# Performance work log

Hardware: AMD Instinct MI355X
Metric: run time of the kernel (lower is better)

## Reference

```python
import jax, jax.numpy as jnp
import numpy as np

N_HEADS = 12
HIDDEN = 768
HEAD_DIM = HIDDEN // N_HEADS
B, S = 4, 2048


def setup_inputs() -> dict:
    key = jax.random.key(0)
    ks = jax.random.split(key, 7)
    bound = 1.0 / np.sqrt(HIDDEN)  # torch nn.Linear default init range
    inputs = jax.random.normal(ks[0], (B, S, HIDDEN), dtype=jnp.float32)
    Wq = jax.random.uniform(ks[1], (HIDDEN, HIDDEN), jnp.float32, -bound, bound)
    bq = jax.random.uniform(ks[2], (HIDDEN,), jnp.float32, -bound, bound)
    Wk = jax.random.uniform(ks[3], (HIDDEN, HIDDEN), jnp.float32, -bound, bound)
    bk = jax.random.uniform(ks[4], (HIDDEN,), jnp.float32, -bound, bound)
    Wv = jax.random.uniform(ks[5], (HIDDEN, HIDDEN), jnp.float32, -bound, bound)
    bv = jax.random.uniform(ks[6], (HIDDEN,), jnp.float32, -bound, bound)
    return {"inputs": inputs, "Wq": Wq, "bq": bq, "Wk": Wk, "bk": bk, "Wv": Wv, "bv": bv}


def reference(inputs, Wq, bq, Wk, bk, Wv, bv):
    b, s, d = inputs.shape
    h, hd = N_HEADS, HEAD_DIM
    # torch Linear: x @ W^T + b; reshape to (b, s, h, hd) -> (b, h, s, hd)
    def proj(W, bias):
        y = inputs @ W.T + bias
        return y.reshape(b, s, h, hd).transpose(0, 2, 1, 3)
    q = proj(Wq, bq)
    k = proj(Wk, bk)
    v = proj(Wv, bv)
    scale = 1.0 / jnp.sqrt(jnp.asarray(hd, inputs.dtype))
    scores = jnp.einsum('bhqd,bhkd->bhqk', q, k) * scale  # [b,h,s,s] materialized as in source
    attn = jax.nn.softmax(scores, axis=-1)
    out = jnp.einsum('bhqk,bhkd->bhqd', attn, v)
    # (b, h, s, hd) -> (b, s, h*hd)
    return out.transpose(0, 2, 1, 3).reshape(b, s, d)
```

## Files before the change

kernel.cpp:

```cpp
#include <hip/hip_runtime.h>
#include <hip/hip_bf16.h>
#include <math.h>

#define NH   12
#define HD   64
#define HID  768
#define NB   4
#define SS   2048
#define MR   (NB*SS)

#define NXE  (MR*HID)
#define NWE  (HID*HID)

typedef unsigned short u16;
typedef u16   u16x8  __attribute__((ext_vector_type(8)));
typedef __bf16 bf16x8 __attribute__((ext_vector_type(8)));
typedef float f32x4  __attribute__((ext_vector_type(4)));

__device__ __forceinline__ u16 f2b(float f) {
    union { float f; unsigned i; } c; c.f = f;
    unsigned x = c.i + 0x7fffu + ((c.i >> 16) & 1u);
    return (u16)(x >> 16);
}
__device__ __forceinline__ unsigned pk2(float lo, float hi) {
    float2 f; f.x = lo; f.y = hi;
    union { __hip_bfloat162 h; unsigned u; } c;
    c.h = __float22bfloat162_rn(f);
    return c.u;
}
__device__ __forceinline__ f32x4 mfma16(u16x8 a, u16x8 b, f32x4 c) {
    return __builtin_amdgcn_mfma_f32_16x16x32_bf16(
        __builtin_bit_cast(bf16x8, a), __builtin_bit_cast(bf16x8, b), c, 0, 0, 0);
}
__device__ __forceinline__ void g2l16(const u16* g, u16* l) {
    __builtin_amdgcn_global_load_lds(
        (const __attribute__((address_space(1))) void*)g,
        (__attribute__((address_space(3))) void*)l, 16, 0, 0);
}
__device__ __forceinline__ int kperm(int k) {
    return ((k >> 5) << 5) | (((k >> 2) & 1) << 4) | (((k >> 3) & 3) << 2) | (k & 3);
}


__global__ __launch_bounds__(256) void to_bf16(
    const float* __restrict__ x,  const float* __restrict__ Wq,
    const float* __restrict__ Wk, const float* __restrict__ Wv,
    u16* __restrict__ dst)
{
    const int NX4 = NXE / 4, NW4 = NWE / 4, NT4 = NX4 + 3 * NW4;
    for (int i = blockIdx.x * 256 + threadIdx.x; i < NT4; i += gridDim.x * 256) {
        const float* src; u16* d;
        if (i < NX4) { src = x + (size_t)i * 4; d = dst + (size_t)i * 4; }
        else {
            int j = i - NX4; int w = j / NW4; int r = j - w * NW4;
            const float* Ws = (w == 0) ? Wq : ((w == 1) ? Wk : Wv);
            src = Ws + (size_t)r * 4; d = dst + NXE + (size_t)w * NWE + (size_t)r * 4;
        }
        float4 f = *(const float4*)src;
        uint2 o; o.x = pk2(f.x, f.y); o.y = pk2(f.z, f.w);
        *(uint2*)d = o;
    }
}

__global__ __launch_bounds__(256, 3) void qkv_proj(
    const u16* __restrict__ xb, const u16* __restrict__ Wb,
    const float* __restrict__ bq, const float* __restrict__ bk,
    const float* __restrict__ bv, u16* __restrict__ qkv)
{
    const int wsel = blockIdx.z;
    const u16* W = Wb + (size_t)wsel * NWE;
    const float* bias = (wsel == 0) ? bq : ((wsel == 1) ? bk : bv);
    u16* out = qkv + (size_t)wsel * MR * HID;

    const int m0 = blockIdx.x * 128, n0 = blockIdx.y * 128;
    __shared__ __align__(16) u16 smem[18432];

    const int tid  = threadIdx.x;
    const int lane = tid & 63, wid = tid >> 6;
    const int quad = lane >> 4, l16 = lane & 15;
    const int wm = wid >> 1, wn = wid & 1;
    const int qsw = quad ^ ((l16 >> 1) & 3);

    const int rA = 2 * wid * 16 + (lane >> 2);
    const int colh = 8 * ((lane & 3) ^ ((lane >> 3) & 3));
    const u16* gx0 = xb + (size_t)(m0 + rA) * HID + colh;
    const u16* gx1 = gx0 + (size_t)16 * HID;
    const u16* gw0 = W  + (size_t)(n0 + rA) * HID + colh;
    const u16* gw1 = gw0 + (size_t)16 * HID;
    u16* lA = smem + (2 * wid) * 512 + lane * 8;

    f32x4 acc[4][4] = {};

    for (int k0 = 0; k0 < HID; k0 += 64) {
        g2l16(gx0 + k0,      lA);            g2l16(gx1 + k0,      lA + 512);
        g2l16(gx0 + k0 + 32, lA + 4096);     g2l16(gx1 + k0 + 32, lA + 4608);
        g2l16(gw0 + k0,      lA + 8192);     g2l16(gw1 + k0,      lA + 8704);
        g2l16(gw0 + k0 + 32, lA + 12288);    g2l16(gw1 + k0 + 32, lA + 12800);
        __syncthreads();
        #pragma unroll
        for (int hh = 0; hh < 2; hh++) {
            u16x8 af[4], bf[4];
            #pragma unroll
            for (int i = 0; i < 4; i++)
                af[i] = *(const u16x8*)(smem + hh * 4096 + (wm * 64 + i * 16 + l16) * 32 + qsw * 8);
            #pragma unroll
            for (int j = 0; j < 4; j++)
                bf[j] = *(const u16x8*)(smem + 8192 + hh * 4096 + (wn * 64 + j * 16 + l16) * 32 + qsw * 8);
            #pragma unroll
            for (int i = 0; i < 4; i++)
                #pragma unroll
                for (int j = 0; j < 4; j++)
                    acc[i][j] = mfma16(af[i], bf[j], acc[i][j]);
        }
        __syncthreads();
    }

    u16* lt = smem + wid * 4608;

    if (wsel == 2) {
        #pragma unroll
        for (int j = 0; j < 4; j++) {
            const int col = n0 + wn * 64 + j * 16 + l16;
            const float bb = bias[col];
            #pragma unroll
            for (int i = 0; i < 4; i++) {
                uint2 pk;
                pk.x = pk2(acc[i][j][0] + bb, acc[i][j][1] + bb);
                pk.y = pk2(acc[i][j][2] + bb, acc[i][j][3] + bb);
                *(uint2*)(lt + (j * 16 + l16) * 72 + i * 16 + quad * 4) = pk;
            }
        }
        __syncthreads();
        const int bidx = m0 >> 11;
        const int s0 = (m0 & 2047) + wm * 64;
        #pragma unroll
        for (int it = 0; it < 8; it++) {
            const int dl = it * 8 + (lane >> 3), sl = (lane & 7) * 8;
            uint4 w = *(const uint4*)(lt + dl * 72 + sl);
            const int col = n0 + wn * 64 + dl;
            const int hh = col >> 6, d = col & 63;
            *(uint4*)(out + ((size_t)(bidx * NH + hh) * HD + d) * SS + s0 + sl) = w;
        }
    } else {
        const float scale = (wsel == 0) ? 0.18033688f : 1.0f;
        #pragma unroll
        for (int j = 0; j < 4; j++) {
            const int col = n0 + wn * 64 + j * 16 + l16;
            const float bb = bias[col];
            #pragma unroll
            for (int i = 0; i < 4; i++)
                #pragma unroll
                for (int r = 0; r < 4; r++)
                    lt[(i * 16 + quad * 4 + r) * 72 + j * 16 + l16] =
                        f2b((acc[i][j][r] + bb) * scale);
        }
        __syncthreads();
        const size_t rowbase = (size_t)(m0 + wm * 64);
        const int cb = n0 + wn * 64;
        #pragma unroll
        for (int it = 0; it < 8; it++) {
            const int dl = it * 8 + (lane >> 3), sl = (lane & 7) * 8;
            uint4 w = *(const uint4*)(lt + dl * 72 + sl);
            const int grow = (wsel == 1) ? kperm(dl) : dl;
            *(uint4*)(out + (rowbase + grow) * HID + cb + sl) = w;
        }
    }
}

__global__ __launch_bounds__(256, 3) void attn(
    const u16* __restrict__ qkv, float* __restrict__ out)
{
    const int lin = blockIdx.x;
    const int rx  = lin & 7;
    const int gg  = lin >> 3;
    const int qt  = gg & 15;
    const int bh  = rx * 6 + (gg >> 4);
    const int b   = bh / NH, h = bh - b * NH;
    const int q0  = qt * 128;

    const u16* qb  = qkv + (size_t)b * SS * HID + h * HD;
    const u16* kb  = qkv + (size_t)MR * HID + (size_t)b * SS * HID + h * HD;
    const u16* vtb = qkv + (size_t)2 * MR * HID + ((size_t)(b * NH + h) * HD) * SS;
    float*     ob  = out + (size_t)b * SS * HID + h * HD;

    __shared__ __align__(16) u16 KS[3][2][2048];
    __shared__ __align__(16) u16 VS[3][2][2048];

    const int tid  = threadIdx.x;
    const int lane = tid & 63, wid = tid >> 6;
    const int quad = lane >> 4, l16 = lane & 15;
    const int qsw = quad ^ ((l16 >> 1) & 3);

    const int srow = 16 * wid + (lane >> 2);
    const int sc8  = 8 * ((lane & 3) ^ ((lane >> 3) & 3));
    const int ldst = wid * 512 + lane * 8;

    const u16* kg = kb + (size_t)srow * HID + sc8;
    const u16* vg = vtb + (size_t)srow * SS + sc8;

#define ASTAGE(kt, bf_) do {                                            \
        const u16* k_ = kg + (size_t)(kt) * 64 * HID;                   \
        const u16* v_ = vg + (kt) * 64;                                 \
        g2l16(k_,      &KS[(bf_)][0][0] + ldst);                        \
        g2l16(k_ + 32, &KS[(bf_)][1][0] + ldst);                        \
        g2l16(v_,      &VS[(bf_)][0][0] + ldst);                        \
        g2l16(v_ + 32, &VS[(bf_)][1][0] + ldst);                        \
    } while (0)

    u16x8 qf[2][2];
    #pragma unroll
    for (int t = 0; t < 2; t++) {
        const int row = q0 + t * 64 + wid * 16 + l16;
        #pragma unroll
        for (int hh = 0; hh < 2; hh++)
            qf[t][hh] = *(const u16x8*)(qb + (size_t)row * HID + hh * 32 + quad * 8);
    }

    u16x8 ones;
    #pragma unroll
    for (int e = 0; e < 8; e++) ones[e] = 0x3F80;

    f32x4 o2[2][4] = {};
    f32x4 lacc[2] = {};

    ASTAGE(0, 0);
    ASTAGE(1, 1);

    for (int kt = 0; kt < SS / 64; kt++) {
        const int cur = kt % 3, nb = (kt + 2) % 3;

        if (kt < 31) asm volatile("s_waitcnt vmcnt(4)" ::: "memory");
        else         asm volatile("s_waitcnt vmcnt(0)" ::: "memory");
        __builtin_amdgcn_s_barrier();
        if (kt + 2 < 32) ASTAGE(kt + 2, nb);

        const u16* ksb = &KS[cur][0][0];
        const u16* vsb = &VS[cur][0][0];

        u16x8 kf[4][2];
        #pragma unroll
        for (int n = 0; n < 4; n++)
            #pragma unroll
            for (int hh = 0; hh < 2; hh++)
                kf[n][hh] = *(const u16x8*)(ksb + hh * 2048 + (n * 16 + l16) * 32 + qsw * 8);

        unsigned pkd[2][4][2];
        __builtin_amdgcn_s_setprio(1);
        #pragma unroll
        for (int t = 0; t < 2; t++)
            #pragma unroll
            for (int n = 0; n < 4; n++) {
                f32x4 s = {-6.f, -6.f, -6.f, -6.f};
                s = mfma16(kf[n][0], qf[t][0], s);
                s = mfma16(kf[n][1], qf[t][1], s);
                const float p0 = __builtin_amdgcn_exp2f(s[0]);
                const float p1 = __builtin_amdgcn_exp2f(s[1]);
                const float p2 = __builtin_amdgcn_exp2f(s[2]);
                const float p3 = __builtin_amdgcn_exp2f(s[3]);
                pkd[t][n][0] = pk2(p0, p1);
                pkd[t][n][1] = pk2(p2, p3);
            }
        __builtin_amdgcn_s_setprio(0);

        u16x8 vf[4][2];
        #pragma unroll
        for (int n2 = 0; n2 < 4; n2++)
            #pragma unroll
            for (int hh = 0; hh < 2; hh++)
                vf[n2][hh] = *(const u16x8*)(vsb + hh * 2048 + (n2 * 16 + l16) * 32 + qsw * 8);

        __builtin_amdgcn_s_setprio(1);
        #pragma unroll
        for (int t = 0; t < 2; t++) {
            union { u16x8 v; unsigned d[4]; } bf0, bf1;
            bf0.d[0] = pkd[t][0][0]; bf0.d[1] = pkd[t][0][1];
            bf0.d[2] = pkd[t][1][0]; bf0.d[3] = pkd[t][1][1];
            bf1.d[0] = pkd[t][2][0]; bf1.d[1] = pkd[t][2][1];
            bf1.d[2] = pkd[t][3][0]; bf1.d[3] = pkd[t][3][1];
            lacc[t] = mfma16(ones, bf0.v, lacc[t]);
            lacc[t] = mfma16(ones, bf1.v, lacc[t]);
            #pragma unroll
            for (int n2 = 0; n2 < 4; n2++) {
                o2[t][n2] = mfma16(vf[n2][0], bf0.v, o2[t][n2]);
                o2[t][n2] = mfma16(vf[n2][1], bf1.v, o2[t][n2]);
            }
        }
        __builtin_amdgcn_s_setprio(0);
    }
#undef ASTAGE

    #pragma unroll
    for (int t = 0; t < 2; t++) {
        const float inv = 1.f / lacc[t][0];
        const int q = q0 + t * 64 + wid * 16 + l16;
        #pragma unroll
        for (int n2 = 0; n2 < 4; n2++) {
            f32x4 w = o2[t][n2];
            w[0] *= inv; w[1] *= inv; w[2] *= inv; w[3] *= inv;
            *(f32x4*)(ob + (size_t)q * HID + n2 * 16 + quad * 4) = w;
        }
    }
}

extern "C" void kernel_launch(void* const* d_in, const int* in_sizes, int n_in,
                              void* d_out, int out_size, void* d_ws, size_t ws_size,
                              hipStream_t stream) {
    const float* x  = (const float*)d_in[0];
    const float* Wq = (const float*)d_in[1];
    const float* bq = (const float*)d_in[2];
    const float* Wk = (const float*)d_in[3];
    const float* bk = (const float*)d_in[4];
    const float* Wv = (const float*)d_in[5];
    const float* bv = (const float*)d_in[6];
    float* out = (float*)d_out;
    u16* qkv = (u16*)d_ws;
    u16* cvt = (u16*)d_out;

    to_bf16<<<1024, 256, 0, stream>>>(x, Wq, Wk, Wv, cvt);

    dim3 gp(MR / 128, HID / 128, 3);
    qkv_proj<<<gp, 256, 0, stream>>>(cvt, cvt + NXE, bq, bk, bv, qkv);

    attn<<<768, 256, 0, stream>>>(qkv, out);
}
```

Measured before the change: 182.0 us.

## Split KV tile across wave pairs with LDS reduction of partial outputs

Changes the per-wave work split in the attention kernel. Each pair of waves now handles 64 query rows, and each wave of the pair covers one half of the 64-key tile, instead of every wave covering 32 query rows against all 64 keys. This halves the K and V fragment LDS reads per wave and reuses each K/V fragment across more query rows. The cost is double the Q fragments and output accumulators held in registers per wave, plus an end-of-kernel LDS reduction with extra barriers in which half the waves sit idle during the store.

```diff
diff --git a/kernel.cpp b/kernel.cpp
--- a/kernel.cpp
+++ b/kernel.cpp
@@ -190,6 +190,8 @@
     const int lane = tid & 63, wid = tid >> 6;
     const int quad = lane >> 4, l16 = lane & 15;
     const int qsw = quad ^ ((l16 >> 1) & 3);
+    const int wq = wid >> 1;
+    const int wk = wid & 1;
 
     const int srow = 16 * wid + (lane >> 2);
     const int sc8  = 8 * ((lane & 3) ^ ((lane >> 3) & 3));
@@ -207,10 +209,10 @@
         g2l16(v_ + 32, &VS[(bf_)][1][0] + ldst);                        \
     } while (0)
 
-    u16x8 qf[2][2];
+    u16x8 qf[4][2];
     #pragma unroll
-    for (int t = 0; t < 2; t++) {
-        const int row = q0 + t * 64 + wid * 16 + l16;
+    for (int t = 0; t < 4; t++) {
+        const int row = q0 + wq * 64 + t * 16 + l16;
         #pragma unroll
         for (int hh = 0; hh < 2; hh++)
             qf[t][hh] = *(const u16x8*)(qb + (size_t)row * HID + hh * 32 + quad * 8);
@@ -220,8 +222,8 @@
     #pragma unroll
     for (int e = 0; e < 8; e++) ones[e] = 0x3F80;
 
-    f32x4 o2[2][4] = {};
-    f32x4 lacc[2] = {};
+    f32x4 o2[4][4] = {};
+    f32x4 lacc[4] = {};
 
     ASTAGE(0, 0);
     ASTAGE(1, 1);
@@ -237,19 +239,24 @@
         const u16* ksb = &KS[cur][0][0];
         const u16* vsb = &VS[cur][0][0];
 
-        u16x8 kf[4][2];
-        #pragma unroll
-        for (int n = 0; n < 4; n++)
+        u16x8 kf[2][2];
+        #pragma unroll
+        for (int n = 0; n < 2; n++)
             #pragma unroll
             for (int hh = 0; hh < 2; hh++)
-                kf[n][hh] = *(const u16x8*)(ksb + hh * 2048 + (n * 16 + l16) * 32 + qsw * 8);
-
-        unsigned pkd[2][4][2];
+                kf[n][hh] = *(const u16x8*)(ksb + hh * 2048 + (wk * 32 + n * 16 + l16) * 32 + qsw * 8);
+
+        u16x8 vf[4];
+        #pragma unroll
+        for (int n2 = 0; n2 < 4; n2++)
+            vf[n2] = *(const u16x8*)(vsb + wk * 2048 + (n2 * 16 + l16) * 32 + qsw * 8);
+
+        unsigned pkd[4][2][2];
         __builtin_amdgcn_s_setprio(1);
         #pragma unroll
-        for (int t = 0; t < 2; t++)
-            #pragma unroll
-            for (int n = 0; n < 4; n++) {
+        for (int t = 0; t < 4; t++)
+            #pragma unroll
+            for (int n = 0; n < 2; n++) {
                 f32x4 s = {-6.f, -6.f, -6.f, -6.f};
                 s = mfma16(kf[n][0], qf[t][0], s);
                 s = mfma16(kf[n][1], qf[t][1], s);
@@ -262,42 +269,54 @@
             }
         __builtin_amdgcn_s_setprio(0);
 
-        u16x8 vf[4][2];
-        #pragma unroll
-        for (int n2 = 0; n2 < 4; n2++)
-            #pragma unroll
-            for (int hh = 0; hh < 2; hh++)
-                vf[n2][hh] = *(const u16x8*)(vsb + hh * 2048 + (n2 * 16 + l16) * 32 + qsw * 8);
-
         __builtin_amdgcn_s_setprio(1);
         #pragma unroll
-        for (int t = 0; t < 2; t++) {
-            union { u16x8 v; unsigned d[4]; } bf0, bf1;
-            bf0.d[0] = pkd[t][0][0]; bf0.d[1] = pkd[t][0][1];
-            bf0.d[2] = pkd[t][1][0]; bf0.d[3] = pkd[t][1][1];
-            bf1.d[0] = pkd[t][2][0]; bf1.d[1] = pkd[t][2][1];
-            bf1.d[2] = pkd[t][3][0]; bf1.d[3] = pkd[t][3][1];
-            lacc[t] = mfma16(ones, bf0.v, lacc[t]);
-            lacc[t] = mfma16(ones, bf1.v, lacc[t]);
-            #pragma unroll
-            for (int n2 = 0; n2 < 4; n2++) {
-                o2[t][n2] = mfma16(vf[n2][0], bf0.v, o2[t][n2]);
-                o2[t][n2] = mfma16(vf[n2][1], bf1.v, o2[t][n2]);
-            }
+        for (int t = 0; t < 4; t++) {
+            union { u16x8 v; unsigned d[4]; } bf;
+            bf.d[0] = pkd[t][0][0]; bf.d[1] = pkd[t][0][1];
+            bf.d[2] = pkd[t][1][0]; bf.d[3] = pkd[t][1][1];
+            lacc[t] = mfma16(ones, bf.v, lacc[t]);
+            #pragma unroll
+            for (int n2 = 0; n2 < 4; n2++)
+                o2[t][n2] = mfma16(vf[n2], bf.v, o2[t][n2]);
         }
         __builtin_amdgcn_s_setprio(0);
     }
 #undef ASTAGE
 
-    #pragma unroll
-    for (int t = 0; t < 2; t++) {
-        const float inv = 1.f / lacc[t][0];
-        const int q = q0 + t * 64 + wid * 16 + l16;
-        #pragma unroll
-        for (int n2 = 0; n2 < 4; n2++) {
-            f32x4 w = o2[t][n2];
-            w[0] *= inv; w[1] *= inv; w[2] *= inv; w[3] *= inv;
-            *(f32x4*)(ob + (size_t)q * HID + n2 * 16 + quad * 4) = w;
+    __syncthreads();
+    {
+        float* red = (wq == 0) ? (float*)&KS[0][0][0] : (float*)&VS[0][0][0];
+        float* p = red + lane * 84;
+        if (wk == 1) {
+            #pragma unroll
+            for (int t = 0; t < 4; t++) {
+                #pragma unroll
+                for (int n2 = 0; n2 < 4; n2++)
+                    *(f32x4*)(p + (t * 4 + n2) * 4) = o2[t][n2];
+                *(f32x4*)(p + 64 + t * 4) = lacc[t];
+            }
+        }
+        __syncthreads();
+        if (wk == 0) {
+            #pragma unroll
+            for (int t = 0; t < 4; t++) {
+                #pragma unroll
+                for (int n2 = 0; n2 < 4; n2++)
+                    o2[t][n2] += *(const f32x4*)(p + (t * 4 + n2) * 4);
+                lacc[t] += *(const f32x4*)(p + 64 + t * 4);
+            }
+            #pragma unroll
+            for (int t = 0; t < 4; t++) {
+                const float inv = 1.f / lacc[t][0];
+                const int q = q0 + wq * 64 + t * 16 + l16;
+                #pragma unroll
+                for (int n2 = 0; n2 < 4; n2++) {
+                    f32x4 w = o2[t][n2];
+                    w[0] *= inv; w[1] *= inv; w[2] *= inv; w[3] *= inv;
+                    *(f32x4*)(ob + (size_t)q * HID + n2 * 16 + quad * 4) = w;
+                }
+            }
         }
     }
 }
```

Result: slower. 204.6 us (+12.4%).
